# Optimization experiments

Hardware: AMD Instinct MI355X
Metric: run time of the kernel (lower is better)

## Reference

```python
import jax, jax.numpy as jnp
import numpy as np

D_MODEL = 1024
NUM_HEADS = 16
D_K = D_MODEL // NUM_HEADS
THETA = 10000.0


def _rope(x, pos):
    # x: [B, H, T, d_k], pos: [T]
    inv_freq = 1.0 / (THETA ** (jnp.arange(0, D_K, 2, dtype=jnp.float32) / D_K))  # [d_k/2]
    ang = pos.astype(jnp.float32)[:, None] * inv_freq[None, :]                    # [T, d_k/2]
    cos = jnp.repeat(jnp.cos(ang), 2, axis=-1)                                    # [T, d_k]
    sin = jnp.repeat(jnp.sin(ang), 2, axis=-1)
    x = x.astype(jnp.float32)
    x0 = x[..., ::2]
    x1 = x[..., 1::2]
    rot = jnp.stack((-x1, x0), axis=-1).reshape(x.shape)  # rotate_half, interleaved
    return x * cos + rot * sin


def setup_inputs() -> dict:
    key = jax.random.key(0)
    k1, k2, k3 = jax.random.split(key, 3)
    B, T = 2, 2048
    sigma_qkv = float(np.sqrt(2.0 / (D_MODEL + 3 * D_MODEL)))
    sigma_out = float(np.sqrt(2.0 / (D_MODEL + D_MODEL)))
    return {
        "x": jax.random.normal(k1, (B, T, D_MODEL), dtype=jnp.float32),
        "w_qkv": jax.random.normal(k2, (3 * D_MODEL, D_MODEL), dtype=jnp.float32) * sigma_qkv,
        "w_out": jax.random.normal(k3, (D_MODEL, D_MODEL), dtype=jnp.float32) * sigma_out,
    }


def reference(x, w_qkv, w_out):
    B, T, _ = x.shape
    qkv = jnp.einsum("btd,ed->bte", x, w_qkv)                 # [B, T, 3*D]
    q, k, v = jnp.split(qkv, 3, axis=-1)

    def split_head(t):
        return t.reshape(B, T, NUM_HEADS, D_K).transpose(0, 2, 1, 3)  # [B, H, T, d_k]

    q, k, v = split_head(q), split_head(k), split_head(v)
    pos = jnp.arange(T)
    q = _rope(q, pos)
    k = _rope(k, pos)

    scores = jnp.einsum("bhqd,bhkd->bhqk", q, k) / jnp.sqrt(jnp.float32(D_K))
    causal = jnp.tril(jnp.ones((T, T), dtype=bool))            # True = keep
    scores = jnp.where(causal[None, None], scores, -jnp.inf)
    attn = jax.nn.softmax(scores, axis=-1)
    out = jnp.einsum("bhqk,bhkd->bhqd", attn, v)               # [B, H, T, d_k]
    out = out.transpose(0, 2, 1, 3).reshape(B, T, D_MODEL)
    return jnp.einsum("btd,ed->bte", out, w_out)
```

## Files before the change

kernel.cpp:

```cpp
#include <hip/hip_runtime.h>
#include <cstdint>
#include <cstddef>

#define BB 2
#define TT 2048
#define DMODEL 1024
#define NHEADS 16
#define DK 64

typedef short short8 __attribute__((ext_vector_type(8)));
typedef unsigned short ushort8 __attribute__((ext_vector_type(8)));
typedef float floatx4 __attribute__((ext_vector_type(4)));
typedef _Float16 half4 __attribute__((ext_vector_type(4)));

#define MFMA_PV(A, B, C) __builtin_amdgcn_mfma_f32_16x16x16f16(A, B, C, 0, 0, 0)

__device__ __forceinline__ unsigned short f2bf(float f) {
    uint32_t u = __builtin_bit_cast(uint32_t, f);
    uint32_t r = (u + 0x7FFFu + ((u >> 16) & 1u)) >> 16;
    return (unsigned short)r;
}
__device__ __forceinline__ float bf2f(unsigned short s) {
    uint32_t u = ((uint32_t)s) << 16;
    return __builtin_bit_cast(float, u);
}

#define GLDS16(g, l) __builtin_amdgcn_global_load_lds( \
    (const __attribute__((address_space(1))) void*)(g), \
    (__attribute__((address_space(3))) void*)(l), 16, 0, 0)

__global__ void castk3(const float* __restrict__ x, unsigned short* __restrict__ xb,
                       const float* __restrict__ wq, unsigned short* __restrict__ wqb,
                       const float* __restrict__ wo, unsigned short* __restrict__ wob) {
    int bid = blockIdx.x;
    const float* in;
    unsigned short* out;
    int base;
    if (bid < 4096)       { in = x;  out = xb;  base = bid * 1024; }
    else if (bid < 7168)  { in = wq; out = wqb; base = (bid - 4096) * 1024; }
    else                  { in = wo; out = wob; base = (bid - 7168) * 1024; }
    int i = base + threadIdx.x * 4;
    float4 v = *(const float4*)(in + i);
    ushort4 o;
    o.x = f2bf(v.x); o.y = f2bf(v.y); o.z = f2bf(v.z); o.w = f2bf(v.w);
    *(ushort4*)(out + i) = o;
}

template <typename OUT>
__global__ __launch_bounds__(256)
void gemm_bt(const unsigned short* __restrict__ A, const unsigned short* __restrict__ B,
             OUT* __restrict__ C, int M, int N, int K) {
    __shared__ unsigned short As[128 * 32];
    __shared__ unsigned short Bs[128 * 32];

    const int tid  = threadIdx.x;
    const int lane = tid & 63;
    const int w    = tid >> 6;
    const int wm   = w & 1;
    const int wn   = w >> 1;
    const int quad = lane >> 4;
    const int l16  = lane & 15;

    const int m0 = blockIdx.y * 128;
    const int n0 = blockIdx.x * 128;

    floatx4 acc[4][4];
#pragma unroll
    for (int a = 0; a < 4; a++)
#pragma unroll
        for (int b = 0; b < 4; b++)
            acc[a][b] = (floatx4){0.f, 0.f, 0.f, 0.f};

    const int c0 = w * 128 + lane;
    const int c1 = c0 + 64;
    const int r0 = c0 >> 2, cc0 = (c0 & 3) ^ ((r0 >> 1) & 3);
    const int r1 = c1 >> 2, cc1 = (c1 & 3) ^ ((r1 >> 1) & 3);

    const unsigned short* gA0 = A + (size_t)(m0 + r0) * K + cc0 * 8;
    const unsigned short* gA1 = A + (size_t)(m0 + r1) * K + cc1 * 8;
    const unsigned short* gB0 = B + (size_t)(n0 + r0) * K + cc0 * 8;
    const unsigned short* gB1 = B + (size_t)(n0 + r1) * K + cc1 * 8;

    unsigned short* lA0 = &As[(2 * w + 0) * 512];
    unsigned short* lA1 = &As[(2 * w + 1) * 512];
    unsigned short* lB0 = &Bs[(2 * w + 0) * 512];
    unsigned short* lB1 = &Bs[(2 * w + 1) * 512];

    const int rsw = (l16 >> 1) & 3;

    for (int k0 = 0; k0 < K; k0 += 32) {
        __syncthreads();
        GLDS16(gA0 + k0, lA0);
        GLDS16(gA1 + k0, lA1);
        GLDS16(gB0 + k0, lB0);
        GLDS16(gB1 + k0, lB1);
        __syncthreads();

        short8 af[4], bf[4];
#pragma unroll
        for (int t = 0; t < 4; t++) {
            af[t] = *(const short8*)&As[(wm * 64 + t * 16 + l16) * 32 + (quad ^ rsw) * 8];
            bf[t] = *(const short8*)&Bs[(wn * 64 + t * 16 + l16) * 32 + (quad ^ rsw) * 8];
        }
#pragma unroll
        for (int tm = 0; tm < 4; tm++)
#pragma unroll
            for (int tn = 0; tn < 4; tn++)
                acc[tm][tn] = __builtin_amdgcn_mfma_f32_16x16x32_bf16(
                    af[tm], bf[tn], acc[tm][tn], 0, 0, 0);
    }

#pragma unroll
    for (int tm = 0; tm < 4; tm++) {
#pragma unroll
        for (int tn = 0; tn < 4; tn++) {
#pragma unroll
            for (int r = 0; r < 4; r++) {
                int m = m0 + wm * 64 + tm * 16 + quad * 4 + r;
                int n = n0 + wn * 64 + tn * 16 + l16;
                if constexpr (sizeof(OUT) == 4)
                    C[(size_t)m * N + n] = acc[tm][tn][r];
                else
                    C[(size_t)m * N + n] = f2bf(acc[tm][tn][r]);
            }
        }
    }
}

__global__ __launch_bounds__(512)
void gemm256(const unsigned short* __restrict__ A, const unsigned short* __restrict__ B,
             unsigned short* __restrict__ C, int M, int N, int K) {
    __shared__ unsigned short As[2][2][8192];
    __shared__ unsigned short Bs[2][2][8192];

    const int tid  = threadIdx.x;
    const int lane = tid & 63;
    const int w    = tid >> 6;
    const int wm   = w >> 2;
    const int wn   = w & 3;
    const int quad = lane >> 4;
    const int l16  = lane & 15;

    const int gx  = gridDim.x;
    const int bid = blockIdx.y * gx + blockIdx.x;
    const int cpx = (gx * gridDim.y) >> 3;
    const int wg  = (bid & 7) * cpx + (bid >> 3);
    const int m0  = (wg / gx) * 256;
    const int n0  = (wg % gx) * 256;

    floatx4 acc[8][4];
#pragma unroll
    for (int a = 0; a < 8; a++)
#pragma unroll
        for (int b = 0; b < 4; b++)
            acc[a][b] = (floatx4){0.f, 0.f, 0.f, 0.f};

    const int r1   = tid >> 3;
    const int koff = ((tid & 7) ^ (r1 & 7)) * 8;
    const unsigned short* Ag = A + (size_t)(m0 + r1) * K + koff;
    const unsigned short* Bg = B + (size_t)(n0 + r1) * K + koff;
    const int NT2 = K >> 6;

#define STAGE_A(dd, hh, kt) { \
    GLDS16(Ag + (size_t)((hh) * 128) * K + (kt) * 64,      &As[dd][hh][tid * 8]); \
    GLDS16(Ag + (size_t)((hh) * 128 + 64) * K + (kt) * 64, &As[dd][hh][4096 + tid * 8]); }
#define STAGE_B(dd, hh, kt) { \
    GLDS16(Bg + (size_t)((hh) * 128) * K + (kt) * 64,      &Bs[dd][hh][tid * 8]); \
    GLDS16(Bg + (size_t)((hh) * 128 + 64) * K + (kt) * 64, &Bs[dd][hh][4096 + tid * 8]); }

#define BARRIER() { __builtin_amdgcn_sched_barrier(0); __builtin_amdgcn_s_barrier(); \
                    __builtin_amdgcn_sched_barrier(0); }

    STAGE_B(0, 0, 0); STAGE_B(0, 1, 0);
    STAGE_A(0, 0, 0); STAGE_A(0, 1, 0);
    STAGE_B(1, 0, 1); STAGE_B(1, 1, 1);
    asm volatile("s_waitcnt vmcnt(4)" ::: "memory");
    BARRIER();

    const int c0    = (quad ^ (l16 & 7)) * 8;
    const int bhalf = wn >> 1;
    const int brow0 = (wn & 1) * 64 + l16;

    short8 a[8], b[8];

    for (int it = 0; it < NT2; ++it) {
        const int d = it & 1;

#pragma unroll
        for (int nfl = 0; nfl < 2; nfl++)
#pragma unroll
            for (int ks = 0; ks < 2; ks++)
                b[2 * nfl + ks] = *(const short8*)&Bs[d][bhalf][(brow0 + nfl * 16) * 64 + (c0 ^ (ks * 32))];
#pragma unroll
        for (int mfl = 0; mfl < 4; mfl++)
#pragma unroll
            for (int ks = 0; ks < 2; ks++)
                a[2 * mfl + ks] = *(const short8*)&As[d][wm][(l16 + mfl * 16) * 64 + (c0 ^ (ks * 32))];
        if (it + 1 < NT2) STAGE_A(d ^ 1, 0, it + 1);
        BARRIER();
        __builtin_amdgcn_s_setprio(1);
#pragma unroll
        for (int mfl = 0; mfl < 4; mfl++)
#pragma unroll
            for (int nf = 0; nf < 2; nf++) {
                acc[mfl][nf] = __builtin_amdgcn_mfma_f32_16x16x32_bf16(a[2 * mfl], b[2 * nf], acc[mfl][nf], 0, 0, 0);
                acc[mfl][nf] = __builtin_amdgcn_mfma_f32_16x16x32_bf16(a[2 * mfl + 1], b[2 * nf + 1], acc[mfl][nf], 0, 0, 0);
            }
        __builtin_amdgcn_s_setprio(0);
        BARRIER();

#pragma unroll
        for (int nfl = 0; nfl < 2; nfl++)
#pragma unroll
            for (int ks = 0; ks < 2; ks++)
                b[4 + 2 * nfl + ks] = *(const short8*)&Bs[d][bhalf][(brow0 + 32 + nfl * 16) * 64 + (c0 ^ (ks * 32))];
        if (it + 1 < NT2) STAGE_A(d ^ 1, 1, it + 1);
        BARRIER();
        __builtin_amdgcn_s_setprio(1);
#pragma unroll
        for (int mfl = 0; mfl < 4; mfl++)
#pragma unroll
            for (int nf = 2; nf < 4; nf++) {
                acc[mfl][nf] = __builtin_amdgcn_mfma_f32_16x16x32_bf16(a[2 * mfl], b[2 * nf], acc[mfl][nf], 0, 0, 0);
                acc[mfl][nf] = __builtin_amdgcn_mfma_f32_16x16x32_bf16(a[2 * mfl + 1], b[2 * nf + 1], acc[mfl][nf], 0, 0, 0);
            }
        __builtin_amdgcn_s_setprio(0);
        BARRIER();

#pragma unroll
        for (int mfl = 0; mfl < 4; mfl++)
#pragma unroll
            for (int ks = 0; ks < 2; ks++)
                a[2 * mfl + ks] = *(const short8*)&As[d][wm][(64 + l16 + mfl * 16) * 64 + (c0 ^ (ks * 32))];
        if (it + 2 < NT2) STAGE_B(d, 0, it + 2);
        BARRIER();
        __builtin_amdgcn_s_setprio(1);
#pragma unroll
        for (int mfl = 0; mfl < 4; mfl++)
#pragma unroll
            for (int nf = 0; nf < 2; nf++) {
                acc[4 + mfl][nf] = __builtin_amdgcn_mfma_f32_16x16x32_bf16(a[2 * mfl], b[2 * nf], acc[4 + mfl][nf], 0, 0, 0);
                acc[4 + mfl][nf] = __builtin_amdgcn_mfma_f32_16x16x32_bf16(a[2 * mfl + 1], b[2 * nf + 1], acc[4 + mfl][nf], 0, 0, 0);
            }
        __builtin_amdgcn_s_setprio(0);
        BARRIER();

        if (it + 2 < NT2) STAGE_B(d, 1, it + 2);
        if (it < NT2 - 2) {
            asm volatile("s_waitcnt vmcnt(4)" ::: "memory");
        } else if (it == NT2 - 2) {
            asm volatile("s_waitcnt vmcnt(0)" ::: "memory");
        }
        BARRIER();
        __builtin_amdgcn_s_setprio(1);
#pragma unroll
        for (int mfl = 0; mfl < 4; mfl++)
#pragma unroll
            for (int nf = 2; nf < 4; nf++) {
                acc[4 + mfl][nf] = __builtin_amdgcn_mfma_f32_16x16x32_bf16(a[2 * mfl], b[2 * nf], acc[4 + mfl][nf], 0, 0, 0);
                acc[4 + mfl][nf] = __builtin_amdgcn_mfma_f32_16x16x32_bf16(a[2 * mfl + 1], b[2 * nf + 1], acc[4 + mfl][nf], 0, 0, 0);
            }
        __builtin_amdgcn_s_setprio(0);
        BARRIER();
    }
#undef STAGE_A
#undef STAGE_B
#undef BARRIER

#pragma unroll
    for (int mf = 0; mf < 8; mf++) {
#pragma unroll
        for (int nf = 0; nf < 4; nf++) {
#pragma unroll
            for (int r = 0; r < 4; r++) {
                int m = m0 + wm * 128 + mf * 16 + quad * 4 + r;
                int n = n0 + wn * 64 + nf * 16 + l16;
                C[(size_t)m * N + n] = f2bf(acc[mf][nf][r]);
            }
        }
    }
}

__global__ __launch_bounds__(256)
void ropevt(const unsigned short* __restrict__ qkv,
            unsigned short* __restrict__ qb, unsigned short* __restrict__ kb,
            unsigned short* __restrict__ vtb) {
    __shared__ unsigned short tile[64][72];
    const int tid = threadIdx.x;
    const int bh  = blockIdx.y;
    const int b = bh >> 4, h = bh & 15;
    const int t0 = blockIdx.x * 64;

    const float QS = 0.18033688f;
#pragma unroll
    for (int rep = 0; rep < 8; rep++) {
        int idx  = rep * 256 + tid;
        int p    = idx & 31;
        int trow = idx >> 5;
        int t    = t0 + trow;

        size_t src = (size_t)(b * TT + t) * 3072 + h * 64 + 2 * p;
        ushort2 qu = *(const ushort2*)(qkv + src);
        ushort2 ku = *(const ushort2*)(qkv + src + 1024);
        float qx = bf2f(qu.x), qy = bf2f(qu.y);
        float kx = bf2f(ku.x), ky = bf2f(ku.y);

        float invf = __powf(10000.f, -((float)(2 * p)) / 64.f);
        float ang  = (float)t * invf;
        float sn, cs;
        __sincosf(ang, &sn, &cs);

        size_t dst = ((size_t)bh * TT + t) * 64 + 2 * p;
        ushort2 qo, ko;
        qo.x = f2bf((qx * cs - qy * sn) * QS); qo.y = f2bf((qy * cs + qx * sn) * QS);
        ko.x = f2bf(kx * cs - ky * sn); ko.y = f2bf(ky * cs + kx * sn);
        *(ushort2*)(qb + dst) = qo;
        *(ushort2*)(kb + dst) = ko;
    }

    const int row = tid >> 2;
    const unsigned short* src = qkv + ((size_t)(b * TT) + t0 + row) * 3072 + 2048 + h * 64;
    {
        int cb = (tid & 3) * 16;
        ushort8 v0 = *(const ushort8*)(src + cb);
        ushort8 v1 = *(const ushort8*)(src + cb + 8);
#pragma unroll
        for (int i = 0; i < 8; i++) tile[row][cb + i] = v0[i];
#pragma unroll
        for (int i = 0; i < 8; i++) tile[row][cb + 8 + i] = v1[i];
    }
    __syncthreads();

    const int d  = tid >> 2;
    const int tc = tid & 3;
    const int hs = (d & 1) * 4;
    ushort8 o0, o1;
#pragma unroll
    for (int i = 0; i < 8; i++) {
        _Float16 hv = (_Float16)bf2f(tile[tc * 16 + (i ^ hs)][d]);
        o0[i] = __builtin_bit_cast(unsigned short, hv);
    }
#pragma unroll
    for (int i = 0; i < 8; i++) {
        _Float16 hv = (_Float16)bf2f(tile[tc * 16 + 8 + (i ^ hs)][d]);
        o1[i] = __builtin_bit_cast(unsigned short, hv);
    }
    unsigned short* dst = vtb + ((size_t)bh * 64 + d) * TT + t0 + tc * 16;
    *(ushort8*)(dst) = o0;
    *(ushort8*)(dst + 8) = o1;
}

__global__ __launch_bounds__(256, 3)
void attn_mfma(const unsigned short* __restrict__ qb,
               const unsigned short* __restrict__ kb,
               const unsigned short* __restrict__ vtb,
               unsigned short* __restrict__ out) {
    __shared__ unsigned short Ks[3][64 * 64];
    __shared__ unsigned short Vs[3][64 * 64];

    const int tid  = threadIdx.x;
    const int lane = tid & 63;
    const int w    = tid >> 6;
    const int quad = lane >> 4;
    const int l16  = lane & 15;

    const int bh    = blockIdx.x;
    const int qtile = gridDim.y - 1 - blockIdx.y;
    const int q0    = qtile * 64;

    const unsigned short* Qp = qb + ((size_t)bh * TT + q0 + w * 16) * 64;
    const unsigned short* Kp = kb + (size_t)bh * TT * 64;
    const unsigned short* Vp = vtb + (size_t)bh * 64 * TT;

    short8 aq[2];
#pragma unroll
    for (int ks = 0; ks < 2; ks++)
        aq[ks] = *(const short8*)(Qp + (size_t)l16 * 64 + ks * 32 + quad * 8);

    floatx4 Oacc[4];
#pragma unroll
    for (int dt = 0; dt < 4; dt++) Oacc[dt] = (floatx4){0.f, 0.f, 0.f, 0.f};
    float m = -1e30f, l = 0.f;

    const int ntiles = qtile + 1;

#define STAGE(IT, P)                                                                      \
    {                                                                                     \
        const int j0s = (IT) * 64;                                                        \
        _Pragma("unroll")                                                                 \
        for (int rep = 0; rep < 2; rep++) {                                               \
            int c    = rep * 256 + tid;                                                   \
            int row  = c >> 3, sl = c & 7;                                                \
            GLDS16(Kp + (size_t)(j0s + row) * 64 + (sl ^ (row & 7)) * 8, &Ks[P][c * 8]);  \
            GLDS16(Vp + (size_t)row * TT + j0s + (sl ^ ((row >> 1) & 7)) * 8,             \
                   &Vs[P][c * 8]);                                                        \
        }                                                                                 \
    }

    STAGE(0, 0);
    if (ntiles > 1) {
        STAGE(1, 1);
        asm volatile("s_waitcnt vmcnt(4)" ::: "memory");
    } else {
        asm volatile("s_waitcnt vmcnt(0)" ::: "memory");
    }
    __builtin_amdgcn_s_barrier();
    __builtin_amdgcn_sched_barrier(0);

    const int ksw = l16 & 7;
    const int vsw = (l16 >> 1) & 7;
    const int vsub = ((quad & 1) ^ (l16 & 1)) * 4;

    for (int it = 0; it < ntiles; ++it) {
        const int p = it % 3;
        if (it + 2 < ntiles) STAGE(it + 2, (it + 2) % 3);

        floatx4 sacc[4];
#pragma unroll
        for (int nt = 0; nt < 4; nt++) sacc[nt] = (floatx4){0.f, 0.f, 0.f, 0.f};
#pragma unroll
        for (int ks = 0; ks < 2; ks++)
#pragma unroll
            for (int nt = 0; nt < 4; nt++) {
                short8 kf = *(const short8*)&Ks[p][(nt * 16 + l16) * 64 + ((ks * 4 + quad) ^ ksw) * 8];
                sacc[nt] = __builtin_amdgcn_mfma_f32_16x16x32_bf16(kf, aq[ks], sacc[nt], 0, 0, 0);
            }

        if (it == qtile) {
            const int qg = w * 16 + l16;
#pragma unroll
            for (int nt = 0; nt < 4; nt++)
#pragma unroll
                for (int r = 0; r < 4; r++)
                    if (nt * 16 + quad * 4 + r > qg) sacc[nt][r] = -1e30f;
        }

        float mx = sacc[0][0];
#pragma unroll
        for (int nt = 0; nt < 4; nt++)
#pragma unroll
            for (int r = 0; r < 4; r++) mx = fmaxf(mx, sacc[nt][r]);
        mx = fmaxf(mx, __shfl_xor(mx, 16));
        mx = fmaxf(mx, __shfl_xor(mx, 32));
        float mnew  = fmaxf(m, mx);
        float alpha = __builtin_amdgcn_exp2f(m - mnew);
        m = mnew;
        float psum = 0.f;
#pragma unroll
        for (int nt = 0; nt < 4; nt++)
#pragma unroll
            for (int r = 0; r < 4; r++) {
                float pv = __builtin_amdgcn_exp2f(sacc[nt][r] - mnew);
                sacc[nt][r] = pv;
                psum += pv;
            }
        psum += __shfl_xor(psum, 16);
        psum += __shfl_xor(psum, 32);
        l = l * alpha + psum;

#pragma unroll
        for (int dt = 0; dt < 4; dt++)
#pragma unroll
            for (int r = 0; r < 4; r++) Oacc[dt][r] *= alpha;

        half4 bp[4];
#pragma unroll
        for (int nt = 0; nt < 4; nt++) {
            half4 h;
            h[0] = (_Float16)sacc[nt][0];
            h[1] = (_Float16)sacc[nt][1];
            h[2] = (_Float16)sacc[nt][2];
            h[3] = (_Float16)sacc[nt][3];
            bp[nt] = h;
        }

#pragma unroll
        for (int dt = 0; dt < 4; dt++)
#pragma unroll
            for (int nt = 0; nt < 4; nt++) {
                int c = nt * 2 + (quad >> 1);
                half4 vf = *(const half4*)&Vs[p][(dt * 16 + l16) * 64 + (c ^ vsw) * 8 + vsub];
                Oacc[dt] = MFMA_PV(vf, bp[nt], Oacc[dt]);
            }

        if (it + 1 < ntiles) {
            if (it + 2 < ntiles) {
                asm volatile("s_waitcnt vmcnt(4)" ::: "memory");
            } else {
                asm volatile("s_waitcnt vmcnt(0)" ::: "memory");
            }
            __builtin_amdgcn_s_barrier();
            __builtin_amdgcn_sched_barrier(0);
        }
    }
#undef STAGE

    const int b = bh >> 4, h = bh & 15;
    const float inv = 1.f / l;
    const size_t base = ((size_t)(b * TT + q0 + w * 16 + l16)) * DMODEL + h * 64 + quad * 4;
#pragma unroll
    for (int dt = 0; dt < 4; dt++) {
        ushort4 pk;
        pk.x = f2bf(Oacc[dt][0] * inv);
        pk.y = f2bf(Oacc[dt][1] * inv);
        pk.z = f2bf(Oacc[dt][2] * inv);
        pk.w = f2bf(Oacc[dt][3] * inv);
        *(ushort4*)(out + base + dt * 16) = pk;
    }
}

extern "C" void kernel_launch(void* const* d_in, const int* in_sizes, int n_in,
                              void* d_out, int out_size, void* d_ws, size_t ws_size,
                              hipStream_t stream) {
    const float* x     = (const float*)d_in[0];
    const float* w_qkv = (const float*)d_in[1];
    const float* w_out = (const float*)d_in[2];
    float* out = (float*)d_out;

    char* ws = (char*)d_ws;

    unsigned short* xb   = (unsigned short*)(ws);
    unsigned short* wqb  = (unsigned short*)(ws + 8388608);
    unsigned short* wob  = (unsigned short*)(ws + 14680064);
    unsigned short* qkvb = (unsigned short*)(ws + 16777216);
    unsigned short* qb   = (unsigned short*)(ws + 41943040);
    unsigned short* kb   = (unsigned short*)(ws + 50331648);
    unsigned short* vtb  = (unsigned short*)(ws + 58720256);
    unsigned short* attb = (unsigned short*)(ws + 67108864);

    castk3<<<8192, 256, 0, stream>>>(x, xb, w_qkv, wqb, w_out, wob);

    gemm256<<<dim3(3072 / 256, 4096 / 256), 512, 0, stream>>>(
        xb, wqb, qkvb, 4096, 3072, 1024);

    ropevt<<<dim3(TT / 64, BB * NHEADS), 256, 0, stream>>>(qkvb, qb, kb, vtb);

    attn_mfma<<<dim3(BB * NHEADS, TT / 64), 256, 0, stream>>>(qb, kb, vtb, attb);

    gemm_bt<float><<<dim3(1024 / 128, 4096 / 128), 256, 0, stream>>>(
        attb, wob, out, 4096, 1024, 1024);
}
```

Before: 188.3 us.

## Add lazy softmax rescaling, precomputed LDS offsets and MFMA priority in attention loop

The change precomputes global and LDS address offsets outside the attention loop and rotates buffer indices instead of using modulo. It skips the online-softmax rescale of the accumulator unless the running max grows by more than a threshold, replacing per-tile alpha multiplies with a wave-uniform branch. It also converts P to fp16 with packed round-toward-zero conversions and raises wave priority around the MFMA blocks. The lazy rescale risks fp16 overflow in P if the threshold is set badly, and it changes rounding slightly.

```diff
diff --git a/kernel.cpp b/kernel.cpp
--- a/kernel.cpp
+++ b/kernel.cpp
@@ -12,6 +12,7 @@
 typedef unsigned short ushort8 __attribute__((ext_vector_type(8)));
 typedef float floatx4 __attribute__((ext_vector_type(4)));
 typedef _Float16 half4 __attribute__((ext_vector_type(4)));
+typedef float float2v __attribute__((ext_vector_type(2)));
 
 #define MFMA_PV(A, B, C) __builtin_amdgcn_mfma_f32_16x16x16f16(A, B, C, 0, 0, 0)
 
@@ -384,17 +385,21 @@
 
     const int ntiles = qtile + 1;
 
-#define STAGE(IT, P)                                                                      \
-    {                                                                                     \
-        const int j0s = (IT) * 64;                                                        \
-        _Pragma("unroll")                                                                 \
-        for (int rep = 0; rep < 2; rep++) {                                               \
-            int c    = rep * 256 + tid;                                                   \
-            int row  = c >> 3, sl = c & 7;                                                \
-            GLDS16(Kp + (size_t)(j0s + row) * 64 + (sl ^ (row & 7)) * 8, &Ks[P][c * 8]);  \
-            GLDS16(Vp + (size_t)row * TT + j0s + (sl ^ ((row >> 1) & 7)) * 8,             \
-                   &Vs[P][c * 8]);                                                        \
-        }                                                                                 \
+    const int cs0 = tid, cs1 = 256 + tid;
+    const int rK0 = cs0 >> 3, sK0 = cs0 & 7;
+    const int rK1 = cs1 >> 3, sK1 = cs1 & 7;
+    const unsigned short* gk0 = Kp + rK0 * 64 + (sK0 ^ (rK0 & 7)) * 8;
+    const unsigned short* gk1 = Kp + rK1 * 64 + (sK1 ^ (rK1 & 7)) * 8;
+    const unsigned short* gv0 = Vp + (size_t)rK0 * TT + (sK0 ^ ((rK0 >> 1) & 7)) * 8;
+    const unsigned short* gv1 = Vp + (size_t)rK1 * TT + (sK1 ^ ((rK1 >> 1) & 7)) * 8;
+    const int ld0 = cs0 * 8, ld1 = cs1 * 8;
+
+#define STAGE(IT, P)                                      \
+    {                                                     \
+        GLDS16(gk0 + (size_t)(IT) * 4096, &Ks[P][ld0]);   \
+        GLDS16(gv0 + (IT) * 64,           &Vs[P][ld0]);   \
+        GLDS16(gk1 + (size_t)(IT) * 4096, &Ks[P][ld1]);   \
+        GLDS16(gv1 + (IT) * 64,           &Vs[P][ld1]);   \
     }
 
     STAGE(0, 0);
@@ -407,24 +412,38 @@
     __builtin_amdgcn_s_barrier();
     __builtin_amdgcn_sched_barrier(0);
 
-    const int ksw = l16 & 7;
-    const int vsw = (l16 >> 1) & 7;
+    const int ksw  = l16 & 7;
+    const int vsw  = (l16 >> 1) & 7;
     const int vsub = ((quad & 1) ^ (l16 & 1)) * 4;
+    const int kofs0 = (l16 * 64 + ((quad) ^ ksw) * 8) * 2;
+    const int kofs1 = (l16 * 64 + ((4 + quad) ^ ksw) * 8) * 2;
+    const int qh    = quad >> 1;
+    const int vofs0 = (l16 * 64 + ((0 + qh) ^ vsw) * 8 + vsub) * 2;
+    const int vofs1 = (l16 * 64 + ((2 + qh) ^ vsw) * 8 + vsub) * 2;
+    const int vofs2 = (l16 * 64 + ((4 + qh) ^ vsw) * 8 + vsub) * 2;
+    const int vofs3 = (l16 * 64 + ((6 + qh) ^ vsw) * 8 + vsub) * 2;
+
+    int p = 0, p2 = 2;
 
     for (int it = 0; it < ntiles; ++it) {
-        const int p = it % 3;
-        if (it + 2 < ntiles) STAGE(it + 2, (it + 2) % 3);
+        if (it + 2 < ntiles) STAGE(it + 2, p2);
+
+        const char* Kb = (const char*)Ks + p * 8192;
+        const char* Vb = (const char*)Vs + p * 8192;
 
         floatx4 sacc[4];
 #pragma unroll
         for (int nt = 0; nt < 4; nt++) sacc[nt] = (floatx4){0.f, 0.f, 0.f, 0.f};
+
+        __builtin_amdgcn_s_setprio(1);
 #pragma unroll
         for (int ks = 0; ks < 2; ks++)
 #pragma unroll
             for (int nt = 0; nt < 4; nt++) {
-                short8 kf = *(const short8*)&Ks[p][(nt * 16 + l16) * 64 + ((ks * 4 + quad) ^ ksw) * 8];
+                short8 kf = *(const short8*)(Kb + (ks ? kofs1 : kofs0) + nt * 2048);
                 sacc[nt] = __builtin_amdgcn_mfma_f32_16x16x32_bf16(kf, aq[ks], sacc[nt], 0, 0, 0);
             }
+        __builtin_amdgcn_s_setprio(0);
 
         if (it == qtile) {
             const int qg = w * 16 + l16;
@@ -435,53 +454,59 @@
                     if (nt * 16 + quad * 4 + r > qg) sacc[nt][r] = -1e30f;
         }
 
-        float mx = sacc[0][0];
-#pragma unroll
-        for (int nt = 0; nt < 4; nt++)
-#pragma unroll
-            for (int r = 0; r < 4; r++) mx = fmaxf(mx, sacc[nt][r]);
+        float t0_ = fmaxf(fmaxf(sacc[0][0], sacc[0][1]), fmaxf(sacc[0][2], sacc[0][3]));
+        float t1_ = fmaxf(fmaxf(sacc[1][0], sacc[1][1]), fmaxf(sacc[1][2], sacc[1][3]));
+        float t2_ = fmaxf(fmaxf(sacc[2][0], sacc[2][1]), fmaxf(sacc[2][2], sacc[2][3]));
+        float t3_ = fmaxf(fmaxf(sacc[3][0], sacc[3][1]), fmaxf(sacc[3][2], sacc[3][3]));
+        float mx  = fmaxf(fmaxf(t0_, t1_), fmaxf(t2_, t3_));
         mx = fmaxf(mx, __shfl_xor(mx, 16));
         mx = fmaxf(mx, __shfl_xor(mx, 32));
-        float mnew  = fmaxf(m, mx);
-        float alpha = __builtin_amdgcn_exp2f(m - mnew);
-        m = mnew;
+
+        if (__any(mx > m + 8.f)) {
+            float mnew  = fmaxf(m, mx);
+            float alpha = __builtin_amdgcn_exp2f(m - mnew);
+            m = mnew;
+            l *= alpha;
+#pragma unroll
+            for (int dt = 0; dt < 4; dt++)
+#pragma unroll
+                for (int r = 0; r < 4; r++) Oacc[dt][r] *= alpha;
+        }
+
         float psum = 0.f;
 #pragma unroll
         for (int nt = 0; nt < 4; nt++)
 #pragma unroll
             for (int r = 0; r < 4; r++) {
-                float pv = __builtin_amdgcn_exp2f(sacc[nt][r] - mnew);
+                float pv = __builtin_amdgcn_exp2f(sacc[nt][r] - m);
                 sacc[nt][r] = pv;
                 psum += pv;
             }
         psum += __shfl_xor(psum, 16);
         psum += __shfl_xor(psum, 32);
-        l = l * alpha + psum;
-
+        l += psum;
+
+        half4 bp[4];
+#pragma unroll
+        for (int nt = 0; nt < 4; nt++) {
+            float lo = __builtin_bit_cast(float, __builtin_amdgcn_cvt_pkrtz(sacc[nt][0], sacc[nt][1]));
+            float hi = __builtin_bit_cast(float, __builtin_amdgcn_cvt_pkrtz(sacc[nt][2], sacc[nt][3]));
+            float2v f2;
+            f2[0] = lo;
+            f2[1] = hi;
+            bp[nt] = __builtin_bit_cast(half4, f2);
+        }
+
+        __builtin_amdgcn_s_setprio(1);
 #pragma unroll
         for (int dt = 0; dt < 4; dt++)
 #pragma unroll
-            for (int r = 0; r < 4; r++) Oacc[dt][r] *= alpha;
-
-        half4 bp[4];
-#pragma unroll
-        for (int nt = 0; nt < 4; nt++) {
-            half4 h;
-            h[0] = (_Float16)sacc[nt][0];
-            h[1] = (_Float16)sacc[nt][1];
-            h[2] = (_Float16)sacc[nt][2];
-            h[3] = (_Float16)sacc[nt][3];
-            bp[nt] = h;
-        }
-
-#pragma unroll
-        for (int dt = 0; dt < 4; dt++)
-#pragma unroll
             for (int nt = 0; nt < 4; nt++) {
-                int c = nt * 2 + (quad >> 1);
-                half4 vf = *(const half4*)&Vs[p][(dt * 16 + l16) * 64 + (c ^ vsw) * 8 + vsub];
+                const int vo = (nt == 0) ? vofs0 : (nt == 1) ? vofs1 : (nt == 2) ? vofs2 : vofs3;
+                half4 vf = *(const half4*)(Vb + vo + dt * 2048);
                 Oacc[dt] = MFMA_PV(vf, bp[nt], Oacc[dt]);
             }
+        __builtin_amdgcn_s_setprio(0);
 
         if (it + 1 < ntiles) {
             if (it + 2 < ntiles) {
@@ -492,6 +517,8 @@
             __builtin_amdgcn_s_barrier();
             __builtin_amdgcn_sched_barrier(0);
         }
+        p  = (p == 2) ? 0 : p + 1;
+        p2 = (p2 == 2) ? 0 : p2 + 1;
     }
 #undef STAGE
 
```

New measurement: 192.6 us. 1.02x slower.
